# Optimization experiments

Hardware: AMD Instinct MI355X
Metric: run time of the kernel (lower is better)

The kernel has to match this reference:

```python
import jax, jax.numpy as jnp
import numpy as np

B, H, S, D = 2, 16, 2048, 128
NEG = -1.0e9  # matches masked_fill_(-1000000000.0)


def setup_inputs() -> dict:
    key = jax.random.key(0)
    kq, kk, kv = jax.random.split(key, 3)
    Q = jax.random.normal(kq, (B, H, S, D), dtype=jnp.float32)
    K = jax.random.normal(kk, (B, H, S, D), dtype=jnp.float32)
    V = jax.random.normal(kv, (B, H, S, D), dtype=jnp.float32)
    # causal mask: True means masked (filled with -1e9)
    causal = jnp.triu(jnp.ones((S, S), dtype=jnp.bool_), k=1)
    attn_mask = jnp.broadcast_to(causal, (B, H, S, S))
    return {"Q": Q, "K": K, "V": V, "attn_mask": attn_mask}


def reference(Q, K, V, attn_mask):
    d_k = K.shape[-1]
    scale = 1.0 / np.sqrt(d_k).astype(np.float32)
    # [B,H,S,S]
    scores = jnp.einsum('bhqd,bhkd->bhqk', Q, K) * scale
    scores = jnp.where(attn_mask, NEG, scores)
    attn = jax.nn.softmax(scores, axis=-1)
    # dropout p=0.0 -> identity
    context = jnp.einsum('bhqk,bhkd->bhqd', attn, V)
    return context
```

## Files before the change

kernel.cpp:

```cpp
#include <hip/hip_runtime.h>
#include <hip/hip_bf16.h>


#define S_LEN 2048
#define D_DIM 128
#define KTILE 64
#define QSCALE 0.12751743f

typedef __attribute__((ext_vector_type(8)))  short short8;
typedef __attribute__((ext_vector_type(4)))  short short4v;
typedef __attribute__((ext_vector_type(16))) float float16v;

#define KROW 136
#define VROW 72
#define PROW 72
#define KS_OFF 0
#define VT_OFF 8704
#define PS_OFF 17920
#define LDS_SHORTS 27136

static __device__ __forceinline__ short f2bs(float f) {
    union { __hip_bfloat16 h; short s; } u;
    u.h = __float2bfloat16(f);
    return u.s;
}

__global__ __launch_bounds__(128, 1)
void sdpa_causal_kernel(const float* __restrict__ Qg,
                        const float* __restrict__ Kg,
                        const float* __restrict__ Vg,
                        float* __restrict__ Og) {
    __shared__ __align__(16) short lds[LDS_SHORTS];
    short* Ks = lds + KS_OFF;
    short* Vt = lds + VT_OFF;

    const int t   = threadIdx.x;
    const int w   = t >> 6;
    const int l   = t & 63;
    const int l31 = l & 31;
    const int h   = l >> 5;

    short* PsA = lds + PS_OFF + w * 2 * 32 * PROW;
    short* PsB = PsA + 32 * PROW;

    const int id  = blockIdx.x;
    const int a   = id >> 3;
    const int bh  = ((id & 7) << 2) + (a >> 4);
    const int prr = a & 15;
    const int pr  = (a & 32) ? (15 - prr) : prr;
    const int qtA = 31 - pr;
    const int qtB = pr;

    const size_t base = (size_t)bh * S_LEN * D_DIM;
    const int q0A = qtA * 64 + w * 32;
    const int q0B = qtB * 64 + w * 32;

    short8 qaA[8], qaB[8];
    {
        const float* qpA = Qg + base + (size_t)(q0A + l31) * D_DIM + h * 8;
        const float* qpB = Qg + base + (size_t)(q0B + l31) * D_DIM + h * 8;
        for (int kc = 0; kc < 8; ++kc) {
            float4 a0 = *(const float4*)(qpA + kc * 16);
            float4 a1 = *(const float4*)(qpA + kc * 16 + 4);
            float4 b0 = *(const float4*)(qpB + kc * 16);
            float4 b1 = *(const float4*)(qpB + kc * 16 + 4);
            short8 fA, fB;
            fA[0]=f2bs(a0.x*QSCALE); fA[1]=f2bs(a0.y*QSCALE);
            fA[2]=f2bs(a0.z*QSCALE); fA[3]=f2bs(a0.w*QSCALE);
            fA[4]=f2bs(a1.x*QSCALE); fA[5]=f2bs(a1.y*QSCALE);
            fA[6]=f2bs(a1.z*QSCALE); fA[7]=f2bs(a1.w*QSCALE);
            fB[0]=f2bs(b0.x*QSCALE); fB[1]=f2bs(b0.y*QSCALE);
            fB[2]=f2bs(b0.z*QSCALE); fB[3]=f2bs(b0.w*QSCALE);
            fB[4]=f2bs(b1.x*QSCALE); fB[5]=f2bs(b1.y*QSCALE);
            fB[6]=f2bs(b1.z*QSCALE); fB[7]=f2bs(b1.w*QSCALE);
            qaA[kc] = fA; qaB[kc] = fB;
        }
    }

    float16v oA[4], oB[4];
    for (int nb = 0; nb < 4; ++nb)
        for (int r = 0; r < 16; ++r) { oA[nb][r] = 0.f; oB[nb][r] = 0.f; }
    float lsA[16], lsB[16];
    for (int r = 0; r < 16; ++r) { lsA[r] = 0.f; lsB[r] = 0.f; }

    const int kkey = t >> 5;
    const int kd0  = (t & 31) << 2;
    const int vk   = t & 63;
    const int vdb  = (t >> 6) << 4;

    const int ntiles = qtA + 1;

    float4 kreg[16], vreg[16];
    for (int g = 0; g < 16; ++g) {
        kreg[g] = *(const float4*)(Kg + base + (size_t)(kkey + 4*g) * D_DIM + kd0);
        vreg[g] = *(const float4*)(Vg + base + (size_t)vk * D_DIM + 4*(vdb + g));
    }

    for (int kt = 0; kt < ntiles; ++kt) {
        const int kb = kt * KTILE;

        __syncthreads();

        for (int g = 0; g < 16; ++g) {
            short4v ks = { f2bs(kreg[g].x), f2bs(kreg[g].y),
                           f2bs(kreg[g].z), f2bs(kreg[g].w) };
            *(short4v*)&Ks[(kkey + 4*g) * KROW + kd0] = ks;
            const int vd = 4 * (vdb + g);
            Vt[(vd + 0) * VROW + vk] = f2bs(vreg[g].x);
            Vt[(vd + 1) * VROW + vk] = f2bs(vreg[g].y);
            Vt[(vd + 2) * VROW + vk] = f2bs(vreg[g].z);
            Vt[(vd + 3) * VROW + vk] = f2bs(vreg[g].w);
        }

        if (kt + 1 < ntiles) {
            const size_t koff = base + (size_t)(kt + 1) * KTILE * D_DIM;
            for (int g = 0; g < 16; ++g) {
                kreg[g] = *(const float4*)(Kg + koff + (size_t)(kkey + 4*g) * D_DIM + kd0);
                vreg[g] = *(const float4*)(Vg + koff + (size_t)vk * D_DIM + 4*(vdb + g));
            }
        }

        __syncthreads();

        const bool bAct = (kt <= qtB);

        for (int n = 0; n < 2; ++n) {
            const short* kr = &Ks[(n * 32 + l31) * KROW + h * 8];
            float16v sA, sB;
            for (int r = 0; r < 16; ++r) { sA[r] = 0.f; sB[r] = 0.f; }
            for (int kc = 0; kc < 8; ++kc) {
                short8 kf = *(const short8*)&kr[kc * 16];
                sA = __builtin_amdgcn_mfma_f32_32x32x16_bf16(qaA[kc], kf, sA, 0, 0, 0);
                if (bAct)
                    sB = __builtin_amdgcn_mfma_f32_32x32x16_bf16(qaB[kc], kf, sB, 0, 0, 0);
            }
            const int keyb = kb + n * 32;
            if (keyb + 31 > q0A) {
                for (int r = 0; r < 16; ++r) {
                    const int q = q0A + (r & 3) + 8 * (r >> 2) + 4 * h;
                    if (keyb + l31 > q) sA[r] = -INFINITY;
                }
            }
            for (int r = 0; r < 16; ++r) {
                const float p = exp2f(sA[r]);
                lsA[r] += p;
                const int row = (r & 3) + 8 * (r >> 2) + 4 * h;
                PsA[row * PROW + n * 32 + l31] = f2bs(p);
            }
            if (bAct) {
                if (keyb + 31 > q0B) {
                    for (int r = 0; r < 16; ++r) {
                        const int q = q0B + (r & 3) + 8 * (r >> 2) + 4 * h;
                        if (keyb + l31 > q) sB[r] = -INFINITY;
                    }
                }
                for (int r = 0; r < 16; ++r) {
                    const float p = exp2f(sB[r]);
                    lsB[r] += p;
                    const int row = (r & 3) + 8 * (r >> 2) + 4 * h;
                    PsB[row * PROW + n * 32 + l31] = f2bs(p);
                }
            }
        }
        __asm__ volatile("" ::: "memory");

        for (int kc2 = 0; kc2 < 4; ++kc2) {
            short8 paA = *(const short8*)&PsA[l31 * PROW + kc2 * 16 + h * 8];
            short8 paB;
            if (bAct) paB = *(const short8*)&PsB[l31 * PROW + kc2 * 16 + h * 8];
            for (int nb = 0; nb < 4; ++nb) {
                short8 vb = *(const short8*)&Vt[(nb * 32 + l31) * VROW + kc2 * 16 + h * 8];
                oA[nb] = __builtin_amdgcn_mfma_f32_32x32x16_bf16(paA, vb, oA[nb], 0, 0, 0);
                if (bAct)
                    oB[nb] = __builtin_amdgcn_mfma_f32_32x32x16_bf16(paB, vb, oB[nb], 0, 0, 0);
            }
        }
    }

    {
        float invA[16], invB[16];
        for (int r = 0; r < 16; ++r) {
            float sa = lsA[r], sb = lsB[r];
            for (int mask = 1; mask < 32; mask <<= 1) {
                sa += __shfl_xor(sa, mask);
                sb += __shfl_xor(sb, mask);
            }
            invA[r] = 1.0f / sa;
            invB[r] = 1.0f / sb;
        }
        const size_t obA = base + (size_t)q0A * D_DIM;
        const size_t obB = base + (size_t)q0B * D_DIM;
        for (int nb = 0; nb < 4; ++nb)
            for (int r = 0; r < 16; ++r) {
                const int row = (r & 3) + 8 * (r >> 2) + 4 * h;
                Og[obA + (size_t)row * D_DIM + nb * 32 + l31] = oA[nb][r] * invA[r];
                Og[obB + (size_t)row * D_DIM + nb * 32 + l31] = oB[nb][r] * invB[r];
            }
    }
}

extern "C" void kernel_launch(void* const* d_in, const int* in_sizes, int n_in,
                              void* d_out, int out_size, void* d_ws, size_t ws_size,
                              hipStream_t stream) {
    (void)in_sizes; (void)n_in; (void)d_ws; (void)ws_size; (void)out_size;
    const float* Qg = (const float*)d_in[0];
    const float* Kg = (const float*)d_in[1];
    const float* Vg = (const float*)d_in[2];
    float* Og = (float*)d_out;
    sdpa_causal_kernel<<<dim3(512), dim3(128), 0, stream>>>(Qg, Kg, Vg, Og);
}
```

Before: 787.1 us.

## Split paired query tiles across four waves instead of two

Each block now runs 256 threads (four waves). Waves 0-1 handle the long query tile A and waves 2-3 the short tile B, instead of each wave carrying both tiles in registers. This roughly halves per-thread register state (Q fragments, accumulators, prefetch buffers), which could allow two blocks per CU, and it spreads the K/V staging across more threads. The trade-off is imbalance: the B waves go idle once their causal range ends but must still take part in every tile's barriers.

```diff
diff --git a/kernel.cpp b/kernel.cpp
--- a/kernel.cpp
+++ b/kernel.cpp
@@ -25,7 +25,7 @@
     return u.s;
 }
 
-__global__ __launch_bounds__(128, 1)
+__global__ __launch_bounds__(256, 2)
 void sdpa_causal_kernel(const float* __restrict__ Qg,
                         const float* __restrict__ Kg,
                         const float* __restrict__ Vg,
@@ -40,8 +40,7 @@
     const int l31 = l & 31;
     const int h   = l >> 5;
 
-    short* PsA = lds + PS_OFF + w * 2 * 32 * PROW;
-    short* PsB = PsA + 32 * PROW;
+    short* Ps = lds + PS_OFF + w * 32 * PROW;
 
     const int id  = blockIdx.x;
     const int a   = id >> 3;
@@ -51,48 +50,42 @@
     const int qtA = 31 - pr;
     const int qtB = pr;
 
+    const int myqt = (w < 2) ? qtA : qtB;
+    const int q0   = myqt * 64 + (w & 1) * 32;
+
     const size_t base = (size_t)bh * S_LEN * D_DIM;
-    const int q0A = qtA * 64 + w * 32;
-    const int q0B = qtB * 64 + w * 32;
 
-    short8 qaA[8], qaB[8];
+    short8 qa[8];
     {
-        const float* qpA = Qg + base + (size_t)(q0A + l31) * D_DIM + h * 8;
-        const float* qpB = Qg + base + (size_t)(q0B + l31) * D_DIM + h * 8;
+        const float* qp = Qg + base + (size_t)(q0 + l31) * D_DIM + h * 8;
         for (int kc = 0; kc < 8; ++kc) {
-            float4 a0 = *(const float4*)(qpA + kc * 16);
-            float4 a1 = *(const float4*)(qpA + kc * 16 + 4);
-            float4 b0 = *(const float4*)(qpB + kc * 16);
-            float4 b1 = *(const float4*)(qpB + kc * 16 + 4);
-            short8 fA, fB;
-            fA[0]=f2bs(a0.x*QSCALE); fA[1]=f2bs(a0.y*QSCALE);
-            fA[2]=f2bs(a0.z*QSCALE); fA[3]=f2bs(a0.w*QSCALE);
-            fA[4]=f2bs(a1.x*QSCALE); fA[5]=f2bs(a1.y*QSCALE);
-            fA[6]=f2bs(a1.z*QSCALE); fA[7]=f2bs(a1.w*QSCALE);
-            fB[0]=f2bs(b0.x*QSCALE); fB[1]=f2bs(b0.y*QSCALE);
-            fB[2]=f2bs(b0.z*QSCALE); fB[3]=f2bs(b0.w*QSCALE);
-            fB[4]=f2bs(b1.x*QSCALE); fB[5]=f2bs(b1.y*QSCALE);
-            fB[6]=f2bs(b1.z*QSCALE); fB[7]=f2bs(b1.w*QSCALE);
-            qaA[kc] = fA; qaB[kc] = fB;
+            float4 x0 = *(const float4*)(qp + kc * 16);
+            float4 x1 = *(const float4*)(qp + kc * 16 + 4);
+            short8 f;
+            f[0]=f2bs(x0.x*QSCALE); f[1]=f2bs(x0.y*QSCALE);
+            f[2]=f2bs(x0.z*QSCALE); f[3]=f2bs(x0.w*QSCALE);
+            f[4]=f2bs(x1.x*QSCALE); f[5]=f2bs(x1.y*QSCALE);
+            f[6]=f2bs(x1.z*QSCALE); f[7]=f2bs(x1.w*QSCALE);
+            qa[kc] = f;
         }
     }
 
-    float16v oA[4], oB[4];
+    float16v o[4];
     for (int nb = 0; nb < 4; ++nb)
-        for (int r = 0; r < 16; ++r) { oA[nb][r] = 0.f; oB[nb][r] = 0.f; }
-    float lsA[16], lsB[16];
-    for (int r = 0; r < 16; ++r) { lsA[r] = 0.f; lsB[r] = 0.f; }
+        for (int r = 0; r < 16; ++r) o[nb][r] = 0.f;
+    float ls[16];
+    for (int r = 0; r < 16; ++r) ls[r] = 0.f;
 
     const int kkey = t >> 5;
     const int kd0  = (t & 31) << 2;
     const int vk   = t & 63;
-    const int vdb  = (t >> 6) << 4;
+    const int vdb  = (t >> 6) << 3;
 
     const int ntiles = qtA + 1;
 
-    float4 kreg[16], vreg[16];
-    for (int g = 0; g < 16; ++g) {
-        kreg[g] = *(const float4*)(Kg + base + (size_t)(kkey + 4*g) * D_DIM + kd0);
+    float4 kreg[8], vreg[8];
+    for (int g = 0; g < 8; ++g) {
+        kreg[g] = *(const float4*)(Kg + base + (size_t)(kkey + 8*g) * D_DIM + kd0);
         vreg[g] = *(const float4*)(Vg + base + (size_t)vk * D_DIM + 4*(vdb + g));
     }
 
@@ -101,10 +94,10 @@
 
         __syncthreads();
 
-        for (int g = 0; g < 16; ++g) {
+        for (int g = 0; g < 8; ++g) {
             short4v ks = { f2bs(kreg[g].x), f2bs(kreg[g].y),
                            f2bs(kreg[g].z), f2bs(kreg[g].w) };
-            *(short4v*)&Ks[(kkey + 4*g) * KROW + kd0] = ks;
+            *(short4v*)&Ks[(kkey + 8*g) * KROW + kd0] = ks;
             const int vd = 4 * (vdb + g);
             Vt[(vd + 0) * VROW + vk] = f2bs(vreg[g].x);
             Vt[(vd + 1) * VROW + vk] = f2bs(vreg[g].y);
@@ -114,87 +107,62 @@
 
         if (kt + 1 < ntiles) {
             const size_t koff = base + (size_t)(kt + 1) * KTILE * D_DIM;
-            for (int g = 0; g < 16; ++g) {
-                kreg[g] = *(const float4*)(Kg + koff + (size_t)(kkey + 4*g) * D_DIM + kd0);
+            for (int g = 0; g < 8; ++g) {
+                kreg[g] = *(const float4*)(Kg + koff + (size_t)(kkey + 8*g) * D_DIM + kd0);
                 vreg[g] = *(const float4*)(Vg + koff + (size_t)vk * D_DIM + 4*(vdb + g));
             }
         }
 
         __syncthreads();
 
-        const bool bAct = (kt <= qtB);
-
-        for (int n = 0; n < 2; ++n) {
-            const short* kr = &Ks[(n * 32 + l31) * KROW + h * 8];
-            float16v sA, sB;
-            for (int r = 0; r < 16; ++r) { sA[r] = 0.f; sB[r] = 0.f; }
-            for (int kc = 0; kc < 8; ++kc) {
-                short8 kf = *(const short8*)&kr[kc * 16];
-                sA = __builtin_amdgcn_mfma_f32_32x32x16_bf16(qaA[kc], kf, sA, 0, 0, 0);
-                if (bAct)
-                    sB = __builtin_amdgcn_mfma_f32_32x32x16_bf16(qaB[kc], kf, sB, 0, 0, 0);
-            }
-            const int keyb = kb + n * 32;
-            if (keyb + 31 > q0A) {
-                for (int r = 0; r < 16; ++r) {
-                    const int q = q0A + (r & 3) + 8 * (r >> 2) + 4 * h;
-                    if (keyb + l31 > q) sA[r] = -INFINITY;
+        if (kt <= myqt) {
+            for (int n = 0; n < 2; ++n) {
+                const short* kr = &Ks[(n * 32 + l31) * KROW + h * 8];
+                float16v s;
+                for (int r = 0; r < 16; ++r) s[r] = 0.f;
+                for (int kc = 0; kc < 8; ++kc) {
+                    short8 kf = *(const short8*)&kr[kc * 16];
+                    s = __builtin_amdgcn_mfma_f32_32x32x16_bf16(qa[kc], kf, s, 0, 0, 0);
                 }
-            }
-            for (int r = 0; r < 16; ++r) {
-                const float p = exp2f(sA[r]);
-                lsA[r] += p;
-                const int row = (r & 3) + 8 * (r >> 2) + 4 * h;
-                PsA[row * PROW + n * 32 + l31] = f2bs(p);
-            }
-            if (bAct) {
-                if (keyb + 31 > q0B) {
+                const int keyb = kb + n * 32;
+                if (keyb + 31 > q0) {
                     for (int r = 0; r < 16; ++r) {
-                        const int q = q0B + (r & 3) + 8 * (r >> 2) + 4 * h;
-                        if (keyb + l31 > q) sB[r] = -INFINITY;
+                        const int q = q0 + (r & 3) + 8 * (r >> 2) + 4 * h;
+                        if (keyb + l31 > q) s[r] = -INFINITY;
                     }
                 }
                 for (int r = 0; r < 16; ++r) {
-                    const float p = exp2f(sB[r]);
-                    lsB[r] += p;
+                    const float p = exp2f(s[r]);
+                    ls[r] += p;
                     const int row = (r & 3) + 8 * (r >> 2) + 4 * h;
-                    PsB[row * PROW + n * 32 + l31] = f2bs(p);
+                    Ps[row * PROW + n * 32 + l31] = f2bs(p);
                 }
             }
-        }
-        __asm__ volatile("" ::: "memory");
+            __asm__ volatile("" ::: "memory");
 
-        for (int kc2 = 0; kc2 < 4; ++kc2) {
-            short8 paA = *(const short8*)&PsA[l31 * PROW + kc2 * 16 + h * 8];
-            short8 paB;
-            if (bAct) paB = *(const short8*)&PsB[l31 * PROW + kc2 * 16 + h * 8];
-            for (int nb = 0; nb < 4; ++nb) {
-                short8 vb = *(const short8*)&Vt[(nb * 32 + l31) * VROW + kc2 * 16 + h * 8];
-                oA[nb] = __builtin_amdgcn_mfma_f32_32x32x16_bf16(paA, vb, oA[nb], 0, 0, 0);
-                if (bAct)
-                    oB[nb] = __builtin_amdgcn_mfma_f32_32x32x16_bf16(paB, vb, oB[nb], 0, 0, 0);
+            for (int kc2 = 0; kc2 < 4; ++kc2) {
+                short8 pa = *(const short8*)&Ps[l31 * PROW + kc2 * 16 + h * 8];
+                for (int nb = 0; nb < 4; ++nb) {
+                    short8 vb = *(const short8*)&Vt[(nb * 32 + l31) * VROW + kc2 * 16 + h * 8];
+                    o[nb] = __builtin_amdgcn_mfma_f32_32x32x16_bf16(pa, vb, o[nb], 0, 0, 0);
+                }
             }
         }
     }
 
     {
-        float invA[16], invB[16];
+        float inv[16];
         for (int r = 0; r < 16; ++r) {
-            float sa = lsA[r], sb = lsB[r];
-            for (int mask = 1; mask < 32; mask <<= 1) {
-                sa += __shfl_xor(sa, mask);
-                sb += __shfl_xor(sb, mask);
-            }
-            invA[r] = 1.0f / sa;
-            invB[r] = 1.0f / sb;
+            float s = ls[r];
+            for (int mask = 1; mask < 32; mask <<= 1)
+                s += __shfl_xor(s, mask);
+            inv[r] = 1.0f / s;
         }
-        const size_t obA = base + (size_t)q0A * D_DIM;
-        const size_t obB = base + (size_t)q0B * D_DIM;
+        const size_t ob = base + (size_t)q0 * D_DIM;
         for (int nb = 0; nb < 4; ++nb)
             for (int r = 0; r < 16; ++r) {
                 const int row = (r & 3) + 8 * (r >> 2) + 4 * h;
-                Og[obA + (size_t)row * D_DIM + nb * 32 + l31] = oA[nb][r] * invA[r];
-                Og[obB + (size_t)row * D_DIM + nb * 32 + l31] = oB[nb][r] * invB[r];
+                Og[ob + (size_t)row * D_DIM + nb * 32 + l31] = o[nb][r] * inv[r];
             }
     }
 }
@@ -207,5 +175,5 @@
     const float* Kg = (const float*)d_in[1];
     const float* Vg = (const float*)d_in[2];
     float* Og = (float*)d_out;
-    sdpa_causal_kernel<<<dim3(512), dim3(128), 0, stream>>>(Qg, Kg, Vg, Og);
+    sdpa_causal_kernel<<<dim3(512), dim3(256), 0, stream>>>(Qg, Kg, Vg, Og);
 }
```

New measurement: 735.1 us. 1.07x faster.
